# Kernel optimization log

Hardware: AMD Instinct MI355X
Metric: run time of the kernel (lower is better)

The kernel has to match this reference:

```python
import jax, jax.numpy as jnp
import numpy as np

B, S, D, H, HD, L, W, MLP = 1, 4096, 1024, 16, 64, 3, 512, 4096
NB = S // W
EPS = 1e-5

def _layer_norm(x, g, b):
    m = jnp.mean(x, axis=-1, keepdims=True)
    v = jnp.mean(jnp.square(x - m), axis=-1, keepdims=True)
    return (x - m) * jax.lax.rsqrt(v + EPS) * g + b

def _rotate_half(x):
    x1, x2 = jnp.split(x, 2, axis=-1)
    return jnp.concatenate([-x2, x1], axis=-1)

def setup_inputs() -> dict:
    key = jax.random.key(0)
    ks = jax.random.split(key, 12)
    def nrm(k, shape):
        return jax.random.normal(k, shape, jnp.float32) * 0.02
    return {
        'hidden_states': jax.random.normal(ks[0], (B, S, D), jnp.float32),
        'position_ids': jnp.broadcast_to(jnp.arange(S, dtype=jnp.int32), (B, S)),
        'ln1_g': jnp.ones((L, D), jnp.float32), 'ln1_b': jnp.zeros((L, D), jnp.float32),
        'wq': nrm(ks[1], (L, D, D)), 'bq': jnp.zeros((L, D), jnp.float32),
        'wk': nrm(ks[2], (L, D, D)), 'bk': jnp.zeros((L, D), jnp.float32),
        'wv': nrm(ks[3], (L, D, D)), 'bv': jnp.zeros((L, D), jnp.float32),
        'wo': nrm(ks[4], (L, D, D)), 'bo': jnp.zeros((L, D), jnp.float32),
        'ln2_g': jnp.ones((L, D), jnp.float32), 'ln2_b': jnp.zeros((L, D), jnp.float32),
        'w1': nrm(ks[5], (L, D, MLP)), 'b1': jnp.zeros((L, MLP), jnp.float32),
        'w2': nrm(ks[6], (L, MLP, D)), 'b2': jnp.zeros((L, D), jnp.float32),
        'fln_g': jnp.ones((D,), jnp.float32), 'fln_b': jnp.zeros((D,), jnp.float32),
    }

def reference(hidden_states, position_ids, ln1_g, ln1_b, wq, bq, wk, bk, wv, bv,
              wo, bo, ln2_g, ln2_b, w1, b1, w2, b2, fln_g, fln_b):
    # RoPE tables (half-split / LLaMA convention)
    inv_freq = 1.0 / (10000.0 ** (jnp.arange(0, HD, 2, dtype=jnp.float32) / HD))
    ang = position_ids.astype(jnp.float32)[..., None] * inv_freq          # [B,S,HD/2]
    cos = jnp.concatenate([jnp.cos(ang)] * 2, axis=-1)[:, :, None, :]     # [B,S,1,HD]
    sin = jnp.concatenate([jnp.sin(ang)] * 2, axis=-1)[:, :, None, :]

    # causal sliding-window mask over (query-in-block, key-in-2-blocks)
    qi = jnp.arange(W)[:, None]
    kj = jnp.arange(2 * W)[None, :]
    rel = qi + W - kj                                                     # = i - j globally
    base = (rel >= 0) & (rel < W)                                         # [W,2W]
    valid = jnp.ones((NB, 2 * W), bool).at[0, :W].set(False)              # no keys before t=0
    mask = base[None, :, :] & valid[:, None, :]                           # [NB,W,2W]
    scale = HD ** -0.5

    x = hidden_states
    for l in range(L):
        h = _layer_norm(x, ln1_g[l], ln1_b[l])
        q = (h @ wq[l] + bq[l]).reshape(B, S, H, HD)
        k = (h @ wk[l] + bk[l]).reshape(B, S, H, HD)
        v = (h @ wv[l] + bv[l]).reshape(B, S, H, HD)
        q = q * cos + _rotate_half(q) * sin
        k = k * cos + _rotate_half(k) * sin
        qb = q.reshape(B, NB, W, H, HD)
        # keys/values for block b = [block b-1, block b] (pad one block in front)
        kp = jnp.pad(k, ((0, 0), (W, 0), (0, 0), (0, 0)))
        vp = jnp.pad(v, ((0, 0), (W, 0), (0, 0), (0, 0)))
        k2 = jnp.concatenate([kp[:, :-W].reshape(B, NB, W, H, HD),
                              kp[:, W:].reshape(B, NB, W, H, HD)], axis=2)  # [B,NB,2W,H,HD]
        v2 = jnp.concatenate([vp[:, :-W].reshape(B, NB, W, H, HD),
                              vp[:, W:].reshape(B, NB, W, H, HD)], axis=2)
        s = jnp.einsum('bnqhd,bnkhd->bnhqk', qb, k2) * scale              # [B,NB,H,W,2W]
        s = jnp.where(mask[None, :, None, :, :], s, -1e30)
        a = jax.nn.softmax(s, axis=-1)
        o = jnp.einsum('bnhqk,bnkhd->bnqhd', a, v2).reshape(B, S, D)
        x = x + (o @ wo[l] + bo[l])
        h = _layer_norm(x, ln2_g[l], ln2_b[l])
        m = jax.nn.gelu(h @ w1[l] + b1[l], approximate=False) @ w2[l] + b2[l]
        x = x + m
    return _layer_norm(x, fln_g, fln_b)
```

## Files before the change

### kernel.cpp

```cpp
#include <hip/hip_runtime.h>

typedef unsigned short u16;
typedef short s8v __attribute__((ext_vector_type(8)));
typedef float f4v __attribute__((ext_vector_type(4)));

__device__ __forceinline__ float bf2f(u16 u){ return __uint_as_float(((unsigned)u)<<16); }
__device__ __forceinline__ u16 f2bf(float f){
  unsigned u = __float_as_uint(f);
  unsigned r = u + 0x7fffu + ((u>>16)&1u);
  return (u16)(r>>16);
}
__device__ __forceinline__ void gload16(const void* g, void* l){
  __builtin_amdgcn_global_load_lds((const __attribute__((address_space(1))) void*)g,
                                   (__attribute__((address_space(3))) void*)l, 16, 0, 0);
}

struct TJobs {
  const float* src[18];
  u16* dst[18];
  int R[18];
  int C[18];
  int start[19];
};

__global__ __launch_bounds__(256) void transpose_pack(TJobs jb){
  __shared__ float tile[32][33];
  int bid = blockIdx.x;
  int j = 0;
  while (bid >= jb.start[j+1]) j++;
  int t = bid - jb.start[j];
  int C = jb.C[j], R = jb.R[j];
  int ctiles = C >> 5;
  int ty = t / ctiles, tx = t - ty*ctiles;
  const float* src = jb.src[j];
  u16* dst = jb.dst[j];
  int tid = threadIdx.x;
  #pragma unroll
  for (int i=0;i<4;i++){
    int e = tid*4 + i;
    int lr = e >> 5, lc = e & 31;
    tile[lr][lc] = src[(long)(ty*32+lr)*C + tx*32+lc];
  }
  __syncthreads();
  #pragma unroll
  for (int i=0;i<4;i++){
    int e = tid*4 + i;
    int lc = e >> 5, lr = e & 31;
    dst[(long)(tx*32+lc)*R + ty*32+lr] = f2bf(tile[lr][lc]);
  }
}

__global__ __launch_bounds__(256) void pack_bias(const float* __restrict__ bq, const float* __restrict__ bk,
                                                 const float* __restrict__ bv, float* __restrict__ outp){
  int t = blockIdx.x*256 + threadIdx.x;
  if (t >= 3*3072) return;
  int l = t / 3072, c = t - l*3072;
  float v = (c < 1024) ? bq[l*1024+c] : (c < 2048) ? bk[l*1024+c-1024] : bv[l*1024+c-2048];
  outp[t] = v;
}

__global__ __launch_bounds__(256) void rope_table(const int* __restrict__ pos, float* __restrict__ cosT,
                                                  float* __restrict__ sinT){
  int t = blockIdx.x*256 + threadIdx.x;
  int j = t & 31, s = t >> 5;
  float f = expf(-(float)j * 0.28782313662425572f);
  float ang = (float)pos[s] * f;
  cosT[t] = cosf(ang);
  sinT[t] = sinf(ang);
}

__global__ __launch_bounds__(256) void rope_apply(const u16* __restrict__ qkv, const float* __restrict__ cosT,
                                                  const float* __restrict__ sinT, u16* __restrict__ qr,
                                                  u16* __restrict__ kr, u16* __restrict__ vr){
  int t = blockIdx.x*256 + threadIdx.x;
  int j = t & 31, h = (t>>5) & 15, s = t >> 9;
  float c = cosT[(s<<5)+j], sn = sinT[(s<<5)+j];
  long base = (long)s*3072 + h*64 + j;
  long ob   = (long)s*1024 + h*64 + j;
  float q0 = bf2f(qkv[base]),      q1 = bf2f(qkv[base+32]);
  float k0 = bf2f(qkv[base+1024]), k1 = bf2f(qkv[base+1056]);
  qr[ob] = f2bf(q0*c - q1*sn);  qr[ob+32] = f2bf(q1*c + q0*sn);
  kr[ob] = f2bf(k0*c - k1*sn);  kr[ob+32] = f2bf(k1*c + k0*sn);
  vr[ob] = qkv[base+2048];      vr[ob+32] = qkv[base+2080];
}

__device__ __forceinline__ float block_sum(float v, float* red, int tid){
  #pragma unroll
  for (int m=1;m<64;m<<=1) v += __shfl_xor(v, m);
  int w = tid >> 6;
  if ((tid & 63) == 0) red[w] = v;
  __syncthreads();
  float r = red[0]+red[1]+red[2]+red[3];
  __syncthreads();
  return r;
}

template<int OUTF32>
__global__ __launch_bounds__(256) void ln_kernel(const float* __restrict__ x, const float* __restrict__ g,
                                                 const float* __restrict__ b, float* __restrict__ outF,
                                                 u16* __restrict__ outH){
  __shared__ float red[4];
  long row = blockIdx.x;
  int tid = threadIdx.x;
  const float4 xv = *reinterpret_cast<const float4*>(x + row*1024 + tid*4);
  float s = xv.x + xv.y + xv.z + xv.w;
  float mean = block_sum(s, red, tid) * (1.0f/1024.0f);
  float d0 = xv.x-mean, d1 = xv.y-mean, d2 = xv.z-mean, d3 = xv.w-mean;
  float ss = d0*d0 + d1*d1 + d2*d2 + d3*d3;
  float var = block_sum(ss, red, tid) * (1.0f/1024.0f);
  float rstd = rsqrtf(var + 1e-5f);
  int c = tid*4;
  const float4 gv = *reinterpret_cast<const float4*>(g + c);
  const float4 bv = *reinterpret_cast<const float4*>(b + c);
  float y0 = d0*rstd*gv.x + bv.x, y1 = d1*rstd*gv.y + bv.y;
  float y2 = d2*rstd*gv.z + bv.z, y3 = d3*rstd*gv.w + bv.w;
  if (OUTF32){
    float4 o; o.x=y0; o.y=y1; o.z=y2; o.w=y3;
    *reinterpret_cast<float4*>(outF + row*1024 + c) = o;
  } else {
    outH[row*1024 + c+0] = f2bf(y0);
    outH[row*1024 + c+1] = f2bf(y1);
    outH[row*1024 + c+2] = f2bf(y2);
    outH[row*1024 + c+3] = f2bf(y3);
  }
}

template<int EPI>
__global__ __launch_bounds__(256) void gemm_bt(const u16* __restrict__ A, const u16* __restrict__ BT,
                                               const float* __restrict__ bias, const float* __restrict__ resid,
                                               float* __restrict__ outF, u16* __restrict__ outH,
                                               int M, int N, int K){
  __shared__ u16 As[4096];
  __shared__ u16 Bs[4096];
  const int tid = threadIdx.x;
  const int bn = blockIdx.x, bm = blockIdx.y;
  const int w = tid >> 6, lane = tid & 63;
  const int wr = w >> 1, wc = w & 1;
  const int l15 = lane & 15, k8 = (lane >> 4) * 8;

  f4v acc[4][4];
  #pragma unroll
  for (int i=0;i<4;i++)
    #pragma unroll
    for (int j=0;j<4;j++)
      acc[i][j] = (f4v){0.f,0.f,0.f,0.f};

  const int fe = tid * 8;
  const int r0 = fe >> 5, c0 = fe & 31;
  const u16* ga0 = A  + ((long)(bm*128 + r0))*K + c0;
  const u16* gb0 = BT + ((long)(bn*128 + r0))*K + c0;
  const u16* ga1 = ga0 + (long)64*K;
  const u16* gb1 = gb0 + (long)64*K;

  for (int k0 = 0; k0 < K; k0 += 32){
    __syncthreads();
    gload16(ga0 + k0, &As[fe]);
    gload16(ga1 + k0, &As[fe + 2048]);
    gload16(gb0 + k0, &Bs[fe]);
    gload16(gb1 + k0, &Bs[fe + 2048]);
    __syncthreads();
    s8v af[4], bfr[4];
    #pragma unroll
    for (int i=0;i<4;i++){
      af[i]  = *(const s8v*)&As[(wr*64 + i*16 + l15)*32 + k8];
      bfr[i] = *(const s8v*)&Bs[(wc*64 + i*16 + l15)*32 + k8];
    }
    #pragma unroll
    for (int mi=0;mi<4;mi++)
      #pragma unroll
      for (int nf=0;nf<4;nf++)
        acc[mi][nf] = __builtin_amdgcn_mfma_f32_16x16x32_bf16(af[mi], bfr[nf], acc[mi][nf], 0, 0, 0);
  }

  const int r4 = (lane >> 4) * 4;
  #pragma unroll
  for (int mi=0;mi<4;mi++){
    int row = bm*128 + wr*64 + mi*16 + r4;
    #pragma unroll
    for (int nf=0;nf<4;nf++){
      int col = bn*128 + wc*64 + nf*16 + l15;
      float bcol = bias[col];
      #pragma unroll
      for (int r=0;r<4;r++){
        float v = acc[mi][nf][r] + bcol;
        long idx = (long)(row + r)*N + col;
        if (EPI == 0){
          outH[idx] = f2bf(v);
        } else if (EPI == 1){
          outF[idx] = resid[idx] + v;
        } else {
          float gl = 0.5f*v*(1.0f + erff(v*0.70710678118654752f));
          outH[idx] = f2bf(gl);
        }
      }
    }
  }
}

__global__ __launch_bounds__(256) void attn_kernel(const u16* __restrict__ qr, const u16* __restrict__ kr,
                                                   const u16* __restrict__ vr, u16* __restrict__ ao){
  __shared__ u16 Pl[4][1280];
  __shared__ u16 Vl[4][2304];
  const int tid = threadIdx.x, w = tid >> 6, lane = tid & 63;
  const int task = blockIdx.x*4 + w;
  const int head = task >> 7;
  const int q0 = (task & 127) * 32;
  const int l15 = lane & 15, lg = lane >> 4, k8 = lg * 8;

  s8v aq[2][2];
  #pragma unroll
  for (int mi=0;mi<2;mi++)
    #pragma unroll
    for (int kf=0;kf<2;kf++)
      aq[mi][kf] = *(const s8v*)&qr[(long)(q0 + mi*16 + l15)*1024 + head*64 + kf*32 + k8];

  f4v o[2][4];
  #pragma unroll
  for (int i=0;i<2;i++)
    #pragma unroll
    for (int j=0;j<4;j++)
      o[i][j] = (f4v){0.f,0.f,0.f,0.f};
  float mrun[2][4], lrun[2][4];
  #pragma unroll
  for (int i=0;i<2;i++)
    #pragma unroll
    for (int r=0;r<4;r++){ mrun[i][r] = -1e30f; lrun[i][r] = 0.f; }

  const int ktlo = (q0 >= 512) ? ((q0 - 511) >> 5) : 0;
  const int kthi = (q0 + 31) >> 5;

  for (int kt = ktlo; kt <= kthi; ++kt){
    const int k0 = kt * 32;
    #pragma unroll
    for (int t=0;t<4;t++){
      int e = t*64 + lane;
      int r = e >> 3, c8 = (e & 7) * 8;
      *(s8v*)&Vl[w][r*72 + c8] = *(const s8v*)&vr[(long)(k0 + r)*1024 + head*64 + c8];
    }
    s8v bk[2][2];
    #pragma unroll
    for (int nf=0;nf<2;nf++)
      #pragma unroll
      for (int kf=0;kf<2;kf++)
        bk[nf][kf] = *(const s8v*)&kr[(long)(k0 + nf*16 + l15)*1024 + head*64 + kf*32 + k8];
    f4v s[2][2];
    #pragma unroll
    for (int mi=0;mi<2;mi++)
      #pragma unroll
      for (int nf=0;nf<2;nf++){
        f4v z = (f4v){0.f,0.f,0.f,0.f};
        z = __builtin_amdgcn_mfma_f32_16x16x32_bf16(aq[mi][0], bk[nf][0], z, 0,0,0);
        z = __builtin_amdgcn_mfma_f32_16x16x32_bf16(aq[mi][1], bk[nf][1], z, 0,0,0);
        s[mi][nf] = z;
      }
    float alpha[2][4];
    #pragma unroll
    for (int mi=0;mi<2;mi++){
      #pragma unroll
      for (int r=0;r<4;r++){
        int q = q0 + mi*16 + lg*4 + r;
        int kk0 = k0 + l15, kk1 = k0 + 16 + l15;
        bool ok0 = (kk0 <= q) && (q - kk0 < 512);
        bool ok1 = (kk1 <= q) && (q - kk1 < 512);
        float sv0 = ok0 ? s[mi][0][r]*0.125f : -1e30f;
        float sv1 = ok1 ? s[mi][1][r]*0.125f : -1e30f;
        float tm = fmaxf(sv0, sv1);
        tm = fmaxf(tm, __shfl_xor(tm, 1));
        tm = fmaxf(tm, __shfl_xor(tm, 2));
        tm = fmaxf(tm, __shfl_xor(tm, 4));
        tm = fmaxf(tm, __shfl_xor(tm, 8));
        float mnew = fmaxf(mrun[mi][r], tm);
        float al = __expf(mrun[mi][r] - mnew);
        float p0 = ok0 ? __expf(sv0 - mnew) : 0.f;
        float p1 = ok1 ? __expf(sv1 - mnew) : 0.f;
        float rs = p0 + p1;
        rs += __shfl_xor(rs, 1);
        rs += __shfl_xor(rs, 2);
        rs += __shfl_xor(rs, 4);
        rs += __shfl_xor(rs, 8);
        mrun[mi][r] = mnew;
        lrun[mi][r] = lrun[mi][r]*al + rs;
        alpha[mi][r] = al;
        s[mi][0][r] = p0;
        s[mi][1][r] = p1;
      }
      #pragma unroll
      for (int df=0;df<4;df++)
        #pragma unroll
        for (int r=0;r<4;r++)
          o[mi][df][r] *= alpha[mi][r];
    }
    #pragma unroll
    for (int mi=0;mi<2;mi++)
      #pragma unroll
      for (int nf=0;nf<2;nf++)
        #pragma unroll
        for (int r=0;r<4;r++)
          Pl[w][(mi*16 + lg*4 + r)*40 + nf*16 + l15] = f2bf(s[mi][nf][r]);
    s8v ap[2];
    #pragma unroll
    for (int mi=0;mi<2;mi++)
      ap[mi] = *(const s8v*)&Pl[w][(mi*16 + l15)*40 + k8];
    s8v bv[4];
    #pragma unroll
    for (int df=0;df<4;df++){
      #pragma unroll
      for (int i=0;i<8;i++)
        bv[df][i] = (short)Vl[w][(k8 + i)*72 + df*16 + l15];
    }
    #pragma unroll
    for (int mi=0;mi<2;mi++)
      #pragma unroll
      for (int df=0;df<4;df++)
        o[mi][df] = __builtin_amdgcn_mfma_f32_16x16x32_bf16(ap[mi], bv[df], o[mi][df], 0,0,0);
  }
  #pragma unroll
  for (int mi=0;mi<2;mi++)
    #pragma unroll
    for (int df=0;df<4;df++)
      #pragma unroll
      for (int r=0;r<4;r++){
        long row = q0 + mi*16 + lg*4 + r;
        int col = head*64 + df*16 + l15;
        ao[row*1024 + col] = f2bf(o[mi][df][r] / lrun[mi][r]);
      }
}

extern "C" void kernel_launch(void* const* d_in, const int* in_sizes, int n_in,
                              void* d_out, int out_size, void* d_ws, size_t ws_size,
                              hipStream_t stream){
  const float* hidden = (const float*)d_in[0];
  const int*   pos    = (const int*)d_in[1];
  const float* ln1_g  = (const float*)d_in[2];
  const float* ln1_b  = (const float*)d_in[3];
  const float* wq     = (const float*)d_in[4];
  const float* bq     = (const float*)d_in[5];
  const float* wk     = (const float*)d_in[6];
  const float* bk     = (const float*)d_in[7];
  const float* wv     = (const float*)d_in[8];
  const float* bv     = (const float*)d_in[9];
  const float* wo     = (const float*)d_in[10];
  const float* bo     = (const float*)d_in[11];
  const float* ln2_g  = (const float*)d_in[12];
  const float* ln2_b  = (const float*)d_in[13];
  const float* w1     = (const float*)d_in[14];
  const float* b1     = (const float*)d_in[15];
  const float* w2     = (const float*)d_in[16];
  const float* b2     = (const float*)d_in[17];
  const float* fg     = (const float*)d_in[18];
  const float* fb     = (const float*)d_in[19];
  float* out = (float*)d_out;

  char* ws = (char*)d_ws;
  size_t off = 0;
  auto alloc = [&](size_t bytes)->char*{
    char* p = ws + off;
    off = (off + bytes + 255) & ~(size_t)255;
    return p;
  };
  u16*   WQKVT = (u16*)  alloc(3ull*3072*1024*2);
  u16*   WOT   = (u16*)  alloc(3ull*1024*1024*2);
  u16*   W1T   = (u16*)  alloc(3ull*4096*1024*2);
  u16*   W2T   = (u16*)  alloc(3ull*1024*4096*2);
  float* BQKV  = (float*)alloc(3ull*3072*4);
  float* COS   = (float*)alloc(4096ull*32*4);
  float* SIN   = (float*)alloc(4096ull*32*4);
  float* X     = (float*)alloc(4096ull*1024*4);
  u16*   HB    = (u16*)  alloc(4096ull*1024*2);
  u16*   QKV   = (u16*)  alloc(4096ull*3072*2);
  u16*   QR    = (u16*)  alloc(4096ull*1024*2);
  u16*   KR    = (u16*)  alloc(4096ull*1024*2);
  u16*   VR    = (u16*)  alloc(4096ull*1024*2);
  u16*   AO    = (u16*)  alloc(4096ull*1024*2);
  u16*   MB    = (u16*)  alloc(4096ull*4096*2);

  TJobs jb;
  int total = 0, ji = 0;
  for (int l=0;l<3;l++){
    const float* srcs[6] = { wq + (size_t)l*1024*1024, wk + (size_t)l*1024*1024, wv + (size_t)l*1024*1024,
                             wo + (size_t)l*1024*1024, w1 + (size_t)l*1024*4096, w2 + (size_t)l*4096*1024 };
    u16* dsts[6] = { WQKVT + (size_t)l*3072*1024, WQKVT + (size_t)l*3072*1024 + 1024*1024,
                     WQKVT + (size_t)l*3072*1024 + 2048*1024, WOT + (size_t)l*1024*1024,
                     W1T + (size_t)l*4096*1024, W2T + (size_t)l*1024*4096 };
    int Rs[6] = {1024,1024,1024,1024,1024,4096};
    int Cs[6] = {1024,1024,1024,1024,4096,1024};
    for (int k=0;k<6;k++){
      jb.src[ji] = srcs[k]; jb.dst[ji] = dsts[k]; jb.R[ji] = Rs[k]; jb.C[ji] = Cs[k];
      jb.start[ji] = total;
      total += (Rs[k]/32)*(Cs[k]/32);
      ji++;
    }
  }
  jb.start[18] = total;

  transpose_pack<<<total, 256, 0, stream>>>(jb);
  pack_bias<<<36, 256, 0, stream>>>(bq, bk, bv, BQKV);
  rope_table<<<512, 256, 0, stream>>>(pos, COS, SIN);

  for (int l=0;l<3;l++){
    const float* xin = (l == 0) ? hidden : X;
    ln_kernel<0><<<4096, 256, 0, stream>>>(xin, ln1_g + l*1024, ln1_b + l*1024, nullptr, HB);
    gemm_bt<0><<<dim3(24,32), 256, 0, stream>>>(HB, WQKVT + (size_t)l*3072*1024, BQKV + l*3072,
                                                nullptr, nullptr, QKV, 4096, 3072, 1024);
    rope_apply<<<8192, 256, 0, stream>>>(QKV, COS, SIN, QR, KR, VR);
    attn_kernel<<<512, 256, 0, stream>>>(QR, KR, VR, AO);
    gemm_bt<1><<<dim3(8,32), 256, 0, stream>>>(AO, WOT + (size_t)l*1024*1024, bo + l*1024,
                                               xin, X, nullptr, 4096, 1024, 1024);
    ln_kernel<0><<<4096, 256, 0, stream>>>(X, ln2_g + l*1024, ln2_b + l*1024, nullptr, HB);
    gemm_bt<2><<<dim3(32,32), 256, 0, stream>>>(HB, W1T + (size_t)l*4096*1024, b1 + l*4096,
                                                nullptr, nullptr, MB, 4096, 4096, 1024);
    gemm_bt<1><<<dim3(8,32), 256, 0, stream>>>(MB, W2T + (size_t)l*1024*4096, b2 + l*1024,
                                               X, X, nullptr, 4096, 1024, 4096);
  }
  ln_kernel<1><<<4096, 256, 0, stream>>>(X, fg, fb, out, nullptr);
}
```

Before: 1.162 ms.

## Double-buffer GEMM LDS tiles and remap workgroups across XCDs

The GEMM kernel now uses two LDS buffers per operand. It issues the global-to-LDS loads for the next K tile before computing on the current one, and needs one barrier per iteration instead of two. The grid is flattened to 1D and block IDs are remapped so consecutive tiles land on the same XCD (id & 7 grouping), aiming for better L2 reuse. This doubles LDS use, which may lower occupancy. It also relies on the async LDS loads finishing before the barrier.

```diff
diff --git a/kernel.cpp b/kernel.cpp
--- a/kernel.cpp
+++ b/kernel.cpp
@@ -130,10 +130,15 @@
                                                const float* __restrict__ bias, const float* __restrict__ resid,
                                                float* __restrict__ outF, u16* __restrict__ outH,
                                                int M, int N, int K){
-  __shared__ u16 As[4096];
-  __shared__ u16 Bs[4096];
+  __shared__ u16 As[2][4096];
+  __shared__ u16 Bs[2][4096];
   const int tid = threadIdx.x;
-  const int bn = blockIdx.x, bm = blockIdx.y;
+  const int gx = N >> 7;
+  const int nwg = gridDim.x;
+  const int cpx = nwg >> 3;
+  const int sbid = (blockIdx.x & 7) * cpx + (blockIdx.x >> 3);
+  const int bn = sbid % gx, bm = sbid / gx;
+
   const int w = tid >> 6, lane = tid & 63;
   const int wr = w >> 1, wc = w & 1;
   const int l15 = lane & 15, k8 = (lane >> 4) * 8;
@@ -152,24 +157,35 @@
   const u16* ga1 = ga0 + (long)64*K;
   const u16* gb1 = gb0 + (long)64*K;
 
-  for (int k0 = 0; k0 < K; k0 += 32){
-    __syncthreads();
-    gload16(ga0 + k0, &As[fe]);
-    gload16(ga1 + k0, &As[fe + 2048]);
-    gload16(gb0 + k0, &Bs[fe]);
-    gload16(gb1 + k0, &Bs[fe + 2048]);
-    __syncthreads();
+  const int nt = K >> 5;
+  gload16(ga0, &As[0][fe]);
+  gload16(ga1, &As[0][fe + 2048]);
+  gload16(gb0, &Bs[0][fe]);
+  gload16(gb1, &Bs[0][fe + 2048]);
+  __syncthreads();
+
+  int cur = 0;
+  for (int t = 0; t < nt; ++t){
+    if (t + 1 < nt){
+      const int kn = (t + 1) << 5;
+      gload16(ga0 + kn, &As[cur^1][fe]);
+      gload16(ga1 + kn, &As[cur^1][fe + 2048]);
+      gload16(gb0 + kn, &Bs[cur^1][fe]);
+      gload16(gb1 + kn, &Bs[cur^1][fe + 2048]);
+    }
     s8v af[4], bfr[4];
     #pragma unroll
     for (int i=0;i<4;i++){
-      af[i]  = *(const s8v*)&As[(wr*64 + i*16 + l15)*32 + k8];
-      bfr[i] = *(const s8v*)&Bs[(wc*64 + i*16 + l15)*32 + k8];
+      af[i]  = *(const s8v*)&As[cur][(wr*64 + i*16 + l15)*32 + k8];
+      bfr[i] = *(const s8v*)&Bs[cur][(wc*64 + i*16 + l15)*32 + k8];
     }
     #pragma unroll
     for (int mi=0;mi<4;mi++)
       #pragma unroll
       for (int nf=0;nf<4;nf++)
         acc[mi][nf] = __builtin_amdgcn_mfma_f32_16x16x32_bf16(af[mi], bfr[nf], acc[mi][nf], 0, 0, 0);
+    __syncthreads();
+    cur ^= 1;
   }
 
   const int r4 = (lane >> 4) * 4;
@@ -400,17 +416,17 @@
   for (int l=0;l<3;l++){
     const float* xin = (l == 0) ? hidden : X;
     ln_kernel<0><<<4096, 256, 0, stream>>>(xin, ln1_g + l*1024, ln1_b + l*1024, nullptr, HB);
-    gemm_bt<0><<<dim3(24,32), 256, 0, stream>>>(HB, WQKVT + (size_t)l*3072*1024, BQKV + l*3072,
-                                                nullptr, nullptr, QKV, 4096, 3072, 1024);
+    gemm_bt<0><<<24*32, 256, 0, stream>>>(HB, WQKVT + (size_t)l*3072*1024, BQKV + l*3072,
+                                          nullptr, nullptr, QKV, 4096, 3072, 1024);
     rope_apply<<<8192, 256, 0, stream>>>(QKV, COS, SIN, QR, KR, VR);
     attn_kernel<<<512, 256, 0, stream>>>(QR, KR, VR, AO);
-    gemm_bt<1><<<dim3(8,32), 256, 0, stream>>>(AO, WOT + (size_t)l*1024*1024, bo + l*1024,
-                                               xin, X, nullptr, 4096, 1024, 1024);
+    gemm_bt<1><<<8*32, 256, 0, stream>>>(AO, WOT + (size_t)l*1024*1024, bo + l*1024,
+                                         xin, X, nullptr, 4096, 1024, 1024);
     ln_kernel<0><<<4096, 256, 0, stream>>>(X, ln2_g + l*1024, ln2_b + l*1024, nullptr, HB);
-    gemm_bt<2><<<dim3(32,32), 256, 0, stream>>>(HB, W1T + (size_t)l*4096*1024, b1 + l*4096,
-                                                nullptr, nullptr, MB, 4096, 4096, 1024);
-    gemm_bt<1><<<dim3(8,32), 256, 0, stream>>>(MB, W2T + (size_t)l*1024*4096, b2 + l*1024,
-                                               X, X, nullptr, 4096, 1024, 4096);
+    gemm_bt<2><<<32*32, 256, 0, stream>>>(HB, W1T + (size_t)l*4096*1024, b1 + l*4096,
+                                          nullptr, nullptr, MB, 4096, 4096, 1024);
+    gemm_bt<1><<<8*32, 256, 0, stream>>>(MB, W2T + (size_t)l*1024*4096, b2 + l*1024,
+                                         X, X, nullptr, 4096, 1024, 4096);
   }
   ln_kernel<1><<<4096, 256, 0, stream>>>(X, fg, fb, out, nullptr);
 }
```

After: 1.021 ms. 12.1% less time.
